# Kernel tuning notes

Measured on AMD Instinct MI355X. Metric: run time of the kernel, lower is better.

## Reference

```python
import jax, jax.numpy as jnp
import numpy as np

T, B, S = 200, 64, 8
D, R, Z, H = 128, 512, 256, 1024
CCOV, CH = 16, 64
DT = 0.05
LAMBDA = 1.0
LOG2PI = float(np.log(2.0 * np.pi))


def _mlp(x, w1, b1, w2, b2):
    return jax.nn.relu(x @ w1 + b1) @ w2 + b2


def setup_inputs() -> dict:
    key = jax.random.key(0)
    ks = jax.random.split(key, 24)
    sc = 0.02
    inp = {
        "X": jax.random.normal(ks[0], (T, B, D), jnp.float32),
        "M": jax.random.uniform(ks[1], (T, B, D), jnp.float32),
        "cov": jax.random.normal(ks[2], (B, CCOV), jnp.float32),
        "path_h": jax.random.normal(ks[3], (T, B, R), jnp.float32),
        "path_hpos": jax.random.normal(ks[4], (T, B, R), jnp.float32),
        "noise": jax.random.normal(ks[5], (T, B, S, Z), jnp.float32),
        # drift MLP: (R+Z) -> H -> Z (tanh applied in reference)
        "drift_w1": jax.random.normal(ks[6], (R + Z, H), jnp.float32) * sc,
        "drift_b1": jnp.zeros((H,), jnp.float32),
        "drift_w2": jax.random.normal(ks[7], (H, Z), jnp.float32) * sc,
        "drift_b2": jnp.zeros((Z,), jnp.float32),
        # diffusion MLP: R -> H -> Z (exp applied in reference)
        "diff_w1": jax.random.normal(ks[8], (R, H), jnp.float32) * sc,
        "diff_b1": jnp.zeros((H,), jnp.float32),
        "diff_w2": jax.random.normal(ks[9], (H, Z), jnp.float32) * sc,
        "diff_b2": jnp.zeros((Z,), jnp.float32),
        # decoder p MLP: (R+Z) -> H -> D
        "p_w1": jax.random.normal(ks[10], (R + Z, H), jnp.float32) * sc,
        "p_b1": jnp.zeros((H,), jnp.float32),
        "p_w2": jax.random.normal(ks[11], (H, D), jnp.float32) * sc,
        "p_b2": jnp.zeros((D,), jnp.float32),
        # covariates SDE map: CCOV -> CH -> Z (tanh applied in reference)
        "cov_w1": jax.random.normal(ks[12], (CCOV, CH), jnp.float32) * sc,
        "cov_b1": jnp.zeros((CH,), jnp.float32),
        "cov_w2": jax.random.normal(ks[13], (CH, Z), jnp.float32) * sc,
        "cov_b2": jnp.zeros((Z,), jnp.float32),
    }
    return inp


def reference(X, M, cov, path_h, path_hpos, noise,
              drift_w1, drift_b1, drift_w2, drift_b2,
              diff_w1, diff_b1, diff_w2, diff_b2,
              p_w1, p_b1, p_w2, p_b2,
              cov_w1, cov_b1, cov_w2, cov_b2):
    dt = DT
    sqrt_dt = np.sqrt(DT).astype(np.float32)
    nB = X.shape[1]

    # z0: covariates_sde_map(cov) repeated over num_samples -> [B, S, Z]
    z0 = jnp.tanh(_mlp(cov, cov_w1, cov_b1, cov_w2, cov_b2))  # [B, Z]
    z0 = jnp.broadcast_to(z0[:, None, :], (nB, S, Z)) * 1.0  # [B, S, Z]

    def step(z, inp):
        h, hpos, Xt, Mrow, eps = inp
        hb = jnp.broadcast_to(h[:, None, :], (nB, S, R))      # prior hidden
        hpb = jnp.broadcast_to(hpos[:, None, :], (nB, S, R))  # posterior hidden

        prior_drift = 0.1 * jnp.tanh(_mlp(jnp.concatenate([hb, z], -1),
                                          drift_w1, drift_b1, drift_w2, drift_b2))
        poster_drift = 0.1 * jnp.tanh(_mlp(jnp.concatenate([hpb, z], -1),
                                           drift_w1, drift_b1, drift_w2, drift_b2))
        diffusion = jnp.exp(_mlp(hb, diff_w1, diff_b1, diff_w2, diff_b2))

        # Euler-Maruyama with posterior drift (train=True path)
        z_new = z + dt * poster_drift + sqrt_dt * diffusion * eps

        # detached min-max normalization over state dim
        z_max = jax.lax.stop_gradient(jnp.max(z_new, -1, keepdims=True))
        z_min = jax.lax.stop_gradient(jnp.min(z_new, -1, keepdims=True))
        z_new = (z_new - z_min) / (z_max - z_min)

        p = _mlp(jnp.concatenate([hb, z_new], -1), p_w1, p_b1, p_w2, p_b2)  # [B,S,D]

        Mt = jnp.mean(Mrow, -1, keepdims=True)  # [B,1]
        errors = (prior_drift - poster_drift) / diffusion
        kld_t = 0.5 * dt * jnp.sum(jnp.mean(errors ** 2, axis=1)) / nB

        # Gaussian NLL with logvar = 0
        nll = 0.5 * (LOG2PI + (Xt[:, None, :] - p) ** 2)  # [B,S,D]
        recon_t = jnp.mean(jnp.sum(jnp.mean(nll, axis=1) * Mt, axis=-1))
        return z_new, (kld_t, recon_t)

    z_final, (klds, recons) = jax.lax.scan(step, z0, (path_h, path_hpos, X, M, noise))
    loss_kld = jnp.sum(klds)
    loss_recon = jnp.sum(recons)
    loss_total = loss_recon + LAMBDA * loss_kld
    return z_final, loss_total, loss_recon, loss_kld
```

## Files before the change

kernel.cpp:

```cpp
#include <hip/hip_runtime.h>
#include <cstddef>
#include <cstdint>

#define T_STEPS 200
#define BB 64
#define SS 8
#define DD 128
#define RR 512
#define ZZ 256
#define HH 1024
#define DT 0.05f
#define SQRT_DT 0.22360679774997896f
#define LOG2PIF 1.8378770664093453f

typedef __attribute__((ext_vector_type(8))) short bf16x8;
typedef __attribute__((ext_vector_type(8))) unsigned short u16x8;
typedef __attribute__((ext_vector_type(4))) float f32x4;
typedef long f8x8;
#define MFMA __builtin_amdgcn_mfma_f32_16x16x32_bf16
#define MFMA8 __builtin_amdgcn_mfma_f32_16x16x32_fp8_fp8

static __device__ __forceinline__ unsigned short f2bf(float x) {
    unsigned int u = __builtin_bit_cast(unsigned int, x);
    u += 0x7fffu + ((u >> 16) & 1u);
    return (unsigned short)(u >> 16);
}
static __device__ __forceinline__ float bf2f(unsigned short h) {
    unsigned int u = ((unsigned int)h) << 16;
    return __builtin_bit_cast(float, u);
}
static __device__ __forceinline__ float fast_tanh(float x) {
    float e = __expf(2.0f * x);
    return 1.0f - 2.0f / (e + 1.0f);
}
static __device__ __forceinline__ unsigned char f2fp8(float x) {
    unsigned int r = 0;
    asm volatile("v_cvt_pk_fp8_f32 %0, %1, %1" : "+v"(r) : "v"(x));
    return (unsigned char)(r & 0xffu);
}
static __device__ __forceinline__ unsigned int f2fp8x4(float a, float b,
                                                      float c, float d) {
    unsigned int p01 = 0, p23 = 0;
    asm volatile("v_cvt_pk_fp8_f32 %0, %1, %2" : "+v"(p01) : "v"(a), "v"(b));
    asm volatile("v_cvt_pk_fp8_f32 %0, %1, %2" : "+v"(p23) : "v"(c), "v"(d));
    return (p01 & 0xffffu) | (p23 << 16);
}

static __device__ __forceinline__ void bar_lds() {
    asm volatile("s_waitcnt lgkmcnt(0)" ::: "memory");
    __builtin_amdgcn_s_barrier();
    __builtin_amdgcn_sched_barrier(0);
}

__global__ void pack_w(const float* __restrict__ src, int K, int N,
                       unsigned short* __restrict__ dst) {
    int total = (K >> 5) * (N >> 4) * 64;
    int p = blockIdx.x * blockDim.x + threadIdx.x;
    if (p >= total) return;
    int lane = p & 63;
    int ksteps = K >> 5;
    int ks = (p >> 6) % ksteps;
    int nt = p / (ksteps << 6);
    int n = (nt << 4) + (lane & 15);
    int k0 = (ks << 5) + ((lane >> 4) << 3);
    uint4 u4;
    unsigned short* tmp = reinterpret_cast<unsigned short*>(&u4);
    for (int i = 0; i < 8; ++i) tmp[i] = f2bf(src[(size_t)(k0 + i) * N + n]);
    *reinterpret_cast<uint4*>(dst + (size_t)p * 8) = u4;
}

__global__ void pack_w_fp8(const float* __restrict__ src, int K, int N,
                           unsigned char* __restrict__ dst) {
    int total = (K >> 5) * (N >> 4) * 64;
    int p = blockIdx.x * blockDim.x + threadIdx.x;
    if (p >= total) return;
    int lane = p & 63;
    int ksteps = K >> 5;
    int ks = (p >> 6) % ksteps;
    int nt = p / (ksteps << 6);
    int n = (nt << 4) + (lane & 15);
    int k0 = (ks << 5) + ((lane >> 4) << 3);
    unsigned long long acc = 0ull;
    for (int i = 0; i < 8; ++i)
        acc |= (unsigned long long)f2fp8(src[(size_t)(k0 + i) * N + n]) << (8 * i);
    *reinterpret_cast<unsigned long long*>(dst + (size_t)p * 8) = acc;
}

__global__ void mt_kernel(const float* __restrict__ M, float* __restrict__ Mt) {
    int wv = (blockIdx.x * blockDim.x + threadIdx.x) >> 6;
    int lane = threadIdx.x & 63;
    if (wv >= T_STEPS * BB) return;
    const float* row = M + (size_t)wv * DD;
    float s = row[lane] + row[lane + 64];
    for (int off = 32; off; off >>= 1) s += __shfl_down(s, off, 64);
    if (lane == 0) Mt[wv] = s * (1.0f / DD);
}

#define PC_GEMM_1024(Asrc, Bp, biasArr, EMIT)                                    \
    {                                                                            \
        f32x4 acc[16];                                                           \
        f32x4 z4 = {0.f, 0.f, 0.f, 0.f};                                        \
        for (int ntl = 0; ntl < 16; ++ntl) acc[ntl] = z4;                        \
        for (int ks = 0; ks < 16; ++ks) {                                        \
            bf16x8 a = *(const bf16x8*)&Asrc[l][(ks << 5) + (q << 3)];           \
            for (int ntl = 0; ntl < 16; ++ntl) {                                 \
                int ntg = (w << 4) + ntl;                                        \
                bf16x8 bb = *(const bf16x8*)(Bp +                                \
                             (((size_t)ntg * 16 + ks) * 64 + lane) * 8);         \
                acc[ntl] = MFMA(a, bb, acc[ntl], 0, 0, 0);                       \
            }                                                                    \
        }                                                                        \
        for (int ntl = 0; ntl < 16; ++ntl) {                                     \
            int n = (((w << 4) + ntl) << 4) + l;                                 \
            float bv = biasArr[n];                                               \
            for (int i = 0; i < 4; ++i) {                                        \
                int rr = (q << 2) + i;                                           \
                float v = acc[ntl][i] + bv;                                      \
                EMIT;                                                            \
            }                                                                    \
        }                                                                        \
    }

#define SCAN_PERM(n) (((n) & ~127) | (((n) & 15) << 3) | (((n) >> 4) & 7))

__global__ __launch_bounds__(256)
void precompute_kernel(const float* __restrict__ h, const float* __restrict__ hpos,
                       const float* __restrict__ b1d, const float* __restrict__ b1p,
                       const float* __restrict__ b1f, const float* __restrict__ b2f,
                       const unsigned short* __restrict__ W1h_p,
                       const unsigned short* __restrict__ PW1h_p,
                       const unsigned short* __restrict__ DW1_p,
                       const unsigned short* __restrict__ DW2_p,
                       unsigned short* __restrict__ HprojQ,
                       unsigned short* __restrict__ HpprojQ,
                       unsigned short* __restrict__ PprojQ,
                       float* __restrict__ DiffQ) {
    __shared__ unsigned short Ahh[16][RR + 8];
    __shared__ unsigned short Ahp[16][RR + 8];
    __shared__ unsigned short Adh[16][HH + 8];
    const int tid = threadIdx.x;
    const int lane = tid & 63;
    const int w = tid >> 6;
    const int q = lane >> 4;
    const int l = lane & 15;
    const int r0 = blockIdx.x << 4;

    for (int idx = tid; idx < (RR << 4); idx += 256) {
        int r = idx >> 9, c = idx & (RR - 1);
        Ahh[r][c] = f2bf(h[(size_t)(r0 + r) * RR + c]);
        Ahp[r][c] = f2bf(hpos[(size_t)(r0 + r) * RR + c]);
    }
    __syncthreads();

    PC_GEMM_1024(Ahh, W1h_p,  b1d,
                 (HprojQ [(size_t)(r0 + rr) * HH + SCAN_PERM(n)] = f2bf(v)));
    PC_GEMM_1024(Ahp, W1h_p,  b1d,
                 (HpprojQ[(size_t)(r0 + rr) * HH + SCAN_PERM(n)] = f2bf(v)));
    PC_GEMM_1024(Ahh, PW1h_p, b1p, (PprojQ [(size_t)(r0 + rr) * HH + n] = f2bf(v)));
    PC_GEMM_1024(Ahh, DW1_p,  b1f, (Adh[rr][n] = f2bf(fmaxf(v, 0.f))));
    __syncthreads();

    {
        f32x4 acc[4];
        f32x4 z4 = {0.f, 0.f, 0.f, 0.f};
        for (int ntl = 0; ntl < 4; ++ntl) acc[ntl] = z4;
        for (int ks = 0; ks < 32; ++ks) {
            bf16x8 a = *(const bf16x8*)&Adh[l][(ks << 5) + (q << 3)];
            for (int ntl = 0; ntl < 4; ++ntl) {
                int ntg = (w << 2) + ntl;
                bf16x8 bb = *(const bf16x8*)(DW2_p +
                             (((size_t)ntg * 32 + ks) * 64 + lane) * 8);
                acc[ntl] = MFMA(a, bb, acc[ntl], 0, 0, 0);
            }
        }
        for (int ntl = 0; ntl < 4; ++ntl) {
            int n = (((w << 2) + ntl) << 4) + l;
            float bv = b2f[n];
            for (int i = 0; i < 4; ++i) {
                int rr = (q << 2) + i;
                DiffQ[(size_t)(r0 + rr) * ZZ + n] = __expf(acc[ntl][i] + bv);
            }
        }
    }
}

__global__ __launch_bounds__(512, 2)
void scan_kernel(const float* __restrict__ cov, const float* __restrict__ noise,
                 const float* __restrict__ b2d,
                 const float* __restrict__ cw1, const float* __restrict__ cb1,
                 const float* __restrict__ cw2, const float* __restrict__ cb2,
                 const unsigned char* __restrict__ W1z_f8,
                 const unsigned char* __restrict__ W2_f8,
                 const unsigned short* __restrict__ HpprojQ,
                 const unsigned short* __restrict__ HprojQ,
                 const float* __restrict__ DiffQ,
                 unsigned short* __restrict__ zhist,
                 float* __restrict__ out,
                 float* __restrict__ loss) {
    __shared__ __align__(16) long W2L[256][64];
    __shared__ __align__(8) unsigned char Az8[8][272];
    __shared__ __align__(8) unsigned char Ah8[16][1032];
    __shared__ __align__(16) float zf[8][256];
    __shared__ float ch[64];

    const int tid = threadIdx.x;
    const int lane = tid & 63;
    const int w = tid >> 6;
    const int q = lane >> 4;
    const int l = lane & 15;
    const int b = blockIdx.x;

    f8x8 w1r[8][8];
    #pragma unroll
    for (int ntl = 0; ntl < 8; ++ntl)
        #pragma unroll
        for (int ks = 0; ks < 8; ++ks)
            w1r[ntl][ks] = *(const f8x8*)(W1z_f8 +
                ((((size_t)(w * 8 + ntl) * 8 + ks) * 64 + lane) << 3));
    f8x8 w2r[32];
    #pragma unroll
    for (int ks = 0; ks < 32; ++ks)
        w2r[ks] = *(const f8x8*)(W2_f8 +
            ((((size_t)(w * 2) * 32 + ks) * 64 + lane) << 3));
    #pragma unroll
    for (int ks = 0; ks < 32; ++ks)
        W2L[w * 32 + ks][lane] = *(const long*)(W2_f8 +
            ((((size_t)(w * 2 + 1) * 32 + ks) * 64 + lane) << 3));

    if (tid < 64) {
        float s = cb1[tid];
        for (int c = 0; c < 16; ++c) s += cov[b * 16 + c] * cw1[c * 64 + tid];
        ch[tid] = fmaxf(s, 0.f);
    }
    __syncthreads();
    if (tid < ZZ) {
        float v = cb2[tid];
        for (int j = 0; j < 64; ++j) v += ch[j] * cw2[j * ZZ + tid];
        v = fast_tanh(v);
        unsigned short hv = f2bf(v);
        unsigned char zb = f2fp8(v);
        for (int s = 0; s < SS; ++s) {
            zf[s][tid] = v;
            Az8[s][tid] = zb;
            zhist[((size_t)b * SS + s) * ZZ + tid] = hv;
        }
    }

    const int colA = (w << 5) + l;
    const int colB = colA + 16;
    float b2dA = b2d[colA], b2dB = b2d[colB];
    float kacc = 0.f;

    float epsA[4], epsB[4], difA = 0.f, difB = 0.f;
    u16x8 hpr;
#define LOAD_SCALARS(TI)                                                        \
    do {                                                                        \
        const size_t tb_ = (size_t)(TI) * BB + b;                               \
        const unsigned short* ps_ = (q < 2) ? HpprojQ : HprojQ;                 \
        hpr = *(const u16x8*)&ps_[tb_ * HH + (w << 7) + (l << 3)];              \
        if (q < 2) {                                                            \
            _Pragma("unroll")                                                   \
            for (int i = 0; i < 4; ++i) {                                       \
                epsA[i] = noise[((tb_ << 3) + (q << 2) + i) * ZZ + colA];       \
                epsB[i] = noise[((tb_ << 3) + (q << 2) + i) * ZZ + colB];       \
            }                                                                   \
            difA = DiffQ[tb_ * ZZ + colA];                                      \
            difB = DiffQ[tb_ * ZZ + colB];                                      \
        }                                                                       \
    } while (0)

    LOAD_SCALARS(0);
    __syncthreads();

    for (int t = 0; t < T_STEPS; ++t) {
        f8x8 a1f[8];
        #pragma unroll
        for (int ks = 0; ks < 8; ++ks)
            a1f[ks] = *(const f8x8*)&Az8[l & 7][(ks << 5) + (q << 3)];
        #pragma unroll
        for (int h = 0; h < 2; ++h) {
            f32x4 acc[4];
            {
                f32x4 z4 = {0.f, 0.f, 0.f, 0.f};
                #pragma unroll
                for (int j = 0; j < 4; ++j) acc[j] = z4;
            }
            #pragma unroll
            for (int ks = 0; ks < 8; ++ks) {
                #pragma unroll
                for (int j = 0; j < 4; ++j)
                    acc[j] = MFMA8(a1f[ks], w1r[h * 4 + j][ks], acc[j], 0, 0, 0);
            }
            #pragma unroll
            for (int j = 0; j < 4; ++j) {
                int ntl = h * 4 + j;
                int n = (w * 8 + ntl) * 16 + l;
                float hp = bf2f(hpr[ntl]);
                #pragma unroll
                for (int i = 0; i < 4; ++i)
                    Ah8[(q << 2) + i][n] = f2fp8(fmaxf(hp + acc[j][i], 0.f));
            }
        }
        bar_lds();

        f32x4 aA[2], aB[2];
        {
            f32x4 z4 = {0.f, 0.f, 0.f, 0.f};
            aA[0] = z4; aA[1] = z4; aB[0] = z4; aB[1] = z4;
        }
        #pragma unroll
        for (int ks = 0; ks < 32; ++ks) {
            f8x8 a2 = *(const f8x8*)&Ah8[l][(ks << 5) + (q << 3)];
            f8x8 bB = (f8x8)W2L[w * 32 + ks][lane];
            aA[ks & 1] = MFMA8(a2, w2r[ks], aA[ks & 1], 0, 0, 0);
            aB[ks & 1] = MFMA8(a2, bB, aB[ks & 1], 0, 0, 0);
        }
        #pragma unroll
        for (int i = 0; i < 4; ++i) {
            float poA = 0.1f * fast_tanh(aA[0][i] + aA[1][i] + b2dA);
            float poB = 0.1f * fast_tanh(aB[0][i] + aB[1][i] + b2dB);
            float prA = __shfl_xor(poA, 32, 64);
            float prB = __shfl_xor(poB, 32, 64);
            if (q < 2) {
                int s = (q << 2) + i;
                float eA = (prA - poA) / difA;
                float eB = (prB - poB) / difB;
                kacc += eA * eA + eB * eB;
                zf[s][colA] += DT * poA + SQRT_DT * difA * epsA[i];
                zf[s][colB] += DT * poB + SQRT_DT * difB * epsB[i];
            }
        }
        if (t + 1 < T_STEPS) LOAD_SCALARS(t + 1);
        bar_lds();

        {
            float4 vv = *(const float4*)&zf[w][lane << 2];
            float mn = fminf(fminf(vv.x, vv.y), fminf(vv.z, vv.w));
            float mx = fmaxf(fmaxf(vv.x, vv.y), fmaxf(vv.z, vv.w));
            for (int off = 32; off; off >>= 1) {
                mn = fminf(mn, __shfl_xor(mn, off, 64));
                mx = fmaxf(mx, __shfl_xor(mx, off, 64));
            }
            float sc = 1.0f / (mx - mn);
            vv.x = (vv.x - mn) * sc; vv.y = (vv.y - mn) * sc;
            vv.z = (vv.z - mn) * sc; vv.w = (vv.w - mn) * sc;
            *(float4*)&zf[w][lane << 2] = vv;
            *(unsigned int*)&Az8[w][lane << 2] = f2fp8x4(vv.x, vv.y, vv.z, vv.w);
            ushort4 hv4;
            hv4.x = f2bf(vv.x); hv4.y = f2bf(vv.y);
            hv4.z = f2bf(vv.z); hv4.w = f2bf(vv.w);
            size_t zo = ((size_t)(t + 1) * BB + b) * (SS * ZZ) + (size_t)w * ZZ;
            *reinterpret_cast<ushort4*>(zhist + zo + (lane << 2)) = hv4;
        }
        bar_lds();
    }
    __syncthreads();

    for (int idx = tid; idx < SS * ZZ; idx += 512) {
        int s = idx >> 8, n = idx & 255;
        out[((size_t)b * SS + s) * ZZ + n] = zf[s][n];
    }

    for (int off = 32; off; off >>= 1) kacc += __shfl_down(kacc, off, 64);
    if (lane == 0) ch[w] = kacc;
    __syncthreads();
    if (tid == 0) {
        float K = 0.f;
        for (int i = 0; i < 8; ++i) K += ch[i];
        float kc = K * (0.5f * DT / (SS * BB));
        atomicAdd(loss + 0, kc);
        atomicAdd(loss + 2, kc);
    }
#undef LOAD_SCALARS
}

__global__ __launch_bounds__(512, 4)
void post_dec(const unsigned short* __restrict__ zhist,
              const unsigned short* __restrict__ PprojQ,
              const float* __restrict__ X, const float* __restrict__ MtQ,
              const float* __restrict__ b2p,
              const unsigned short* __restrict__ PW1z_p,
              const unsigned short* __restrict__ PW2_p,
              float* __restrict__ loss) {
    __shared__ unsigned short Az[4][16][ZZ + 8];
    __shared__ unsigned short Hp[4][16][136];
    __shared__ unsigned short ProjS[8][128];
    __shared__ float b2p_s[DD];
    __shared__ float red[8];
    const int tid = threadIdx.x;
    const int lane = tid & 63;
    const int w = tid >> 6;
    const int q = lane >> 4;
    const int l = lane & 15;
    const int rt = w & 3;
    const int half = w >> 2;
    const int p0 = blockIdx.x << 3;

    for (int idx = tid; idx < 4096; idx += 512) {
        int r = idx >> 6, c4 = (idx & 63) << 2;
        *(ushort4*)&Az[r >> 4][r & 15][c4] =
            *(const ushort4*)&zhist[((size_t)(p0 + BB) * SS + r) * ZZ + c4];
    }
    if (tid < DD) b2p_s[tid] = b2p[tid];

    f32x4 pacc[4];
    {
        f32x4 z4 = {0.f, 0.f, 0.f, 0.f};
        #pragma unroll
        for (int j = 0; j < 4; ++j) pacc[j] = z4;
    }

    for (int nc = 0; nc < 8; ++nc) {
        if (tid < 256) {
            int pair = tid >> 5, c4 = (tid & 31) << 2;
            *(ushort4*)&ProjS[pair][c4] =
                *(const ushort4*)&PprojQ[(size_t)(p0 + pair) * HH + nc * 128 + c4];
        }
        __syncthreads();

        f32x4 za[4];
        {
            f32x4 z4 = {0.f, 0.f, 0.f, 0.f};
            #pragma unroll
            for (int j = 0; j < 4; ++j) za[j] = z4;
        }
        {
            const unsigned short* wb = PW1z_p + lane * 8;
            bf16x8 wq[4];
            #pragma unroll
            for (int f = 0; f < 4; ++f) {
                int ks = f >> 2, j = f & 3;
                wq[f] = *(const bf16x8*)(wb +
                    ((size_t)((nc * 8 + half * 4 + j) * 8 + ks)) * 512);
            }
            #pragma unroll
            for (int f = 0; f < 32; ++f) {
                int ks = f >> 2, j = f & 3;
                bf16x8 a = *(const bf16x8*)&Az[rt][l][(ks << 5) + (q << 3)];
                za[j] = MFMA(a, wq[f & 3], za[j], 0, 0, 0);
                if (f < 28) {
                    int f2 = f + 4, ks2 = f2 >> 2, j2 = f2 & 3;
                    wq[f & 3] = *(const bf16x8*)(wb +
                        ((size_t)((nc * 8 + half * 4 + j2) * 8 + ks2)) * 512);
                }
            }
        }
        #pragma unroll
        for (int j = 0; j < 4; ++j) {
            int c = (half * 4 + j) * 16 + l;
            #pragma unroll
            for (int i = 0; i < 4; ++i) {
                int r = (q << 2) + i;
                int pair = ((rt << 4) + r) >> 3;
                Hp[rt][r][c] = f2bf(fmaxf(bf2f(ProjS[pair][c]) + za[j][i], 0.f));
            }
        }
        __syncthreads();

        {
            const unsigned short* wb2 = PW2_p + lane * 8;
            bf16x8 wq2[4];
            #pragma unroll
            for (int f = 0; f < 4; ++f) {
                int kk = f >> 2, j = f & 3;
                wq2[f] = *(const bf16x8*)(wb2 +
                    ((size_t)((half * 4 + j) * 32 + nc * 4 + kk)) * 512);
            }
            #pragma unroll
            for (int f = 0; f < 16; ++f) {
                int kk = f >> 2, j = f & 3;
                bf16x8 a = *(const bf16x8*)&Hp[rt][l][(kk << 5) + (q << 3)];
                pacc[j] = MFMA(a, wq2[f & 3], pacc[j], 0, 0, 0);
                if (f < 12) {
                    int f2 = f + 4, kk2 = f2 >> 2, j2 = f2 & 3;
                    wq2[f & 3] = *(const bf16x8*)(wb2 +
                        ((size_t)((half * 4 + j2) * 32 + nc * 4 + kk2)) * 512);
                }
            }
        }
        __syncthreads();
    }

    float rl = 0.f;
    #pragma unroll
    for (int j = 0; j < 4; ++j) {
        int n = ((half << 2) + j) * 16 + l;
        float bias = b2p_s[n];
        #pragma unroll
        for (int i = 0; i < 4; ++i) {
            int r = (rt << 4) + (q << 2) + i;
            int pair = p0 + (r >> 3);
            float p = pacc[j][i] + bias;
            float d = X[(size_t)pair * DD + n] - p;
            rl += (0.5f * (LOG2PIF + d * d)) * MtQ[pair];
        }
    }
    rl *= 1.0f / (SS * BB);
    for (int off = 32; off; off >>= 1) rl += __shfl_down(rl, off, 64);
    if (lane == 0) red[w] = rl;
    __syncthreads();
    if (tid == 0) {
        float R = 0.f;
        for (int i = 0; i < 8; ++i) R += red[i];
        atomicAdd(loss + 0, R);
        atomicAdd(loss + 1, R);
    }
}

extern "C" void kernel_launch(void* const* d_in, const int* in_sizes, int n_in,
                              void* d_out, int out_size, void* d_ws, size_t ws_size,
                              hipStream_t stream) {
    (void)in_sizes; (void)n_in; (void)ws_size;
    const float* X         = (const float*)d_in[0];
    const float* M         = (const float*)d_in[1];
    const float* cov       = (const float*)d_in[2];
    const float* path_h    = (const float*)d_in[3];
    const float* path_hpos = (const float*)d_in[4];
    const float* noise     = (const float*)d_in[5];
    const float* drift_w1  = (const float*)d_in[6];
    const float* drift_b1  = (const float*)d_in[7];
    const float* drift_w2  = (const float*)d_in[8];
    const float* drift_b2  = (const float*)d_in[9];
    const float* diff_w1   = (const float*)d_in[10];
    const float* diff_b1   = (const float*)d_in[11];
    const float* diff_w2   = (const float*)d_in[12];
    const float* diff_b2   = (const float*)d_in[13];
    const float* p_w1      = (const float*)d_in[14];
    const float* p_b1      = (const float*)d_in[15];
    const float* p_w2      = (const float*)d_in[16];
    const float* p_b2      = (const float*)d_in[17];
    const float* cov_w1    = (const float*)d_in[18];
    const float* cov_b1    = (const float*)d_in[19];
    const float* cov_w2    = (const float*)d_in[20];
    const float* cov_b2    = (const float*)d_in[21];

    char* ws = (char*)d_ws;
    size_t off = 0;
    auto alloc = [&](size_t bytes) {
        void* p = ws + off;
        off = (off + bytes + 255) & ~(size_t)255;
        return p;
    };
    unsigned short* HprojQ  = (unsigned short*)alloc((size_t)T_STEPS * BB * HH * 2);
    unsigned short* HpprojQ = (unsigned short*)alloc((size_t)T_STEPS * BB * HH * 2);
    unsigned short* PprojQ  = (unsigned short*)alloc((size_t)T_STEPS * BB * HH * 2);
    float*          DiffQ   = (float*)alloc((size_t)T_STEPS * BB * ZZ * 4);
    float*          MtQ     = (float*)alloc((size_t)T_STEPS * BB * 4);
    unsigned short* zhist   = (unsigned short*)alloc((size_t)(T_STEPS + 1) * BB * SS * ZZ * 2);
    unsigned short* PW1z_p  = (unsigned short*)alloc((size_t)ZZ * HH * 2);
    unsigned short* PW2_p   = (unsigned short*)alloc((size_t)HH * DD * 2);
    unsigned short* W1h_p   = (unsigned short*)alloc((size_t)RR * HH * 2);
    unsigned short* PW1h_p  = (unsigned short*)alloc((size_t)RR * HH * 2);
    unsigned short* DW1_p   = (unsigned short*)alloc((size_t)RR * HH * 2);
    unsigned short* DW2_p   = (unsigned short*)alloc((size_t)HH * ZZ * 2);
    unsigned char*  W1z_f8  = (unsigned char*)alloc((size_t)ZZ * HH);
    unsigned char*  W2_f8   = (unsigned char*)alloc((size_t)HH * ZZ);

    hipMemsetAsync(d_out, 0, (size_t)out_size * sizeof(float), stream);

    auto packLaunch = [&](const float* src, int K, int N, unsigned short* dst) {
        int total = (K / 32) * (N / 16) * 64;
        pack_w<<<(total + 255) / 256, 256, 0, stream>>>(src, K, N, dst);
    };
    auto packLaunch8 = [&](const float* src, int K, int N, unsigned char* dst) {
        int total = (K / 32) * (N / 16) * 64;
        pack_w_fp8<<<(total + 255) / 256, 256, 0, stream>>>(src, K, N, dst);
    };
    packLaunch(p_w1 + (size_t)RR * HH,     ZZ, HH, PW1z_p);
    packLaunch(p_w2,                       HH, DD, PW2_p);
    packLaunch(drift_w1, RR, HH, W1h_p);
    packLaunch(p_w1,     RR, HH, PW1h_p);
    packLaunch(diff_w1,  RR, HH, DW1_p);
    packLaunch(diff_w2,  HH, ZZ, DW2_p);
    packLaunch8(drift_w1 + (size_t)RR * HH, ZZ, HH, W1z_f8);
    packLaunch8(drift_w2,                   HH, ZZ, W2_f8);

    mt_kernel<<<(T_STEPS * BB * 64) / 256, 256, 0, stream>>>(M, MtQ);

    precompute_kernel<<<(T_STEPS * BB) / 16, 256, 0, stream>>>(
        path_h, path_hpos, drift_b1, p_b1, diff_b1, diff_b2,
        W1h_p, PW1h_p, DW1_p, DW2_p, HprojQ, HpprojQ, PprojQ, DiffQ);

    float* outp = (float*)d_out;
    float* loss = outp + (size_t)BB * SS * ZZ;

    scan_kernel<<<BB, 512, 0, stream>>>(
        cov, noise, drift_b2, cov_w1, cov_b1, cov_w2, cov_b2,
        W1z_f8, W2_f8, HpprojQ, HprojQ, DiffQ, zhist, outp, loss);

    post_dec<<<(T_STEPS * BB) / 8, 512, 0, stream>>>(
        zhist, PprojQ, X, MtQ, p_b2, PW1z_p, PW2_p, loss);
}
```

Measured before the change: 1.557 ms.

## Merge scan and decoder into persistent kernel with progress-flag producer/consumer overlap

Fuses the sequential scan kernel and the post-decoder kernel into one launch. 64 blocks run the SDE scan and publish per-batch progress counters every 32 steps, while 192 extra blocks poll those counters and decode/compute the reconstruction loss for completed timesteps concurrently. This hides the decoder work behind the latency-bound scan, at the cost of a larger shared memory footprint (one 158KB buffer for both roles, limiting occupancy). It also relies on all 256 blocks being co-resident; if the consumer blocks spin while producer blocks cannot be scheduled, the kernel could stall.

Measured after the change: 1.554 ms. No clear change (-0.2%).

```diff
diff --git a/kernel.cpp b/kernel.cpp
--- a/kernel.cpp
+++ b/kernel.cpp
@@ -185,7 +185,7 @@
 }
 
 __global__ __launch_bounds__(512, 2)
-void scan_kernel(const float* __restrict__ cov, const float* __restrict__ noise,
+void mega_kernel(const float* __restrict__ cov, const float* __restrict__ noise,
                  const float* __restrict__ b2d,
                  const float* __restrict__ cw1, const float* __restrict__ cb1,
                  const float* __restrict__ cw2, const float* __restrict__ cb2,
@@ -196,63 +196,72 @@
                  const float* __restrict__ DiffQ,
                  unsigned short* __restrict__ zhist,
                  float* __restrict__ out,
-                 float* __restrict__ loss) {
-    __shared__ __align__(16) long W2L[256][64];
-    __shared__ __align__(8) unsigned char Az8[8][272];
-    __shared__ __align__(8) unsigned char Ah8[16][1032];
-    __shared__ __align__(16) float zf[8][256];
-    __shared__ float ch[64];
+                 float* __restrict__ loss,
+                 const unsigned short* __restrict__ PprojQ,
+                 const float* __restrict__ X, const float* __restrict__ MtQ,
+                 const float* __restrict__ b2p,
+                 const unsigned short* __restrict__ PW1z_p,
+                 const unsigned short* __restrict__ PW2_p,
+                 unsigned int* __restrict__ progress) {
+    __shared__ __align__(16) char smem[158208];
 
     const int tid = threadIdx.x;
     const int lane = tid & 63;
     const int w = tid >> 6;
     const int q = lane >> 4;
     const int l = lane & 15;
-    const int b = blockIdx.x;
-
-    f8x8 w1r[8][8];
-    #pragma unroll
-    for (int ntl = 0; ntl < 8; ++ntl)
+
+    if (blockIdx.x < BB) {
+        long (*W2L)[64]            = reinterpret_cast<long(*)[64]>(smem);
+        unsigned char (*Az8)[272]  = reinterpret_cast<unsigned char(*)[272]>(smem + 131072);
+        unsigned char (*Ah8)[1032] = reinterpret_cast<unsigned char(*)[1032]>(smem + 133248);
+        float (*zf)[256]           = reinterpret_cast<float(*)[256]>(smem + 149760);
+        float* ch                  = reinterpret_cast<float*>(smem + 157952);
+        const int b = blockIdx.x;
+
+        f8x8 w1r[8][8];
         #pragma unroll
-        for (int ks = 0; ks < 8; ++ks)
-            w1r[ntl][ks] = *(const f8x8*)(W1z_f8 +
-                ((((size_t)(w * 8 + ntl) * 8 + ks) * 64 + lane) << 3));
-    f8x8 w2r[32];
-    #pragma unroll
-    for (int ks = 0; ks < 32; ++ks)
-        w2r[ks] = *(const f8x8*)(W2_f8 +
-            ((((size_t)(w * 2) * 32 + ks) * 64 + lane) << 3));
-    #pragma unroll
-    for (int ks = 0; ks < 32; ++ks)
-        W2L[w * 32 + ks][lane] = *(const long*)(W2_f8 +
-            ((((size_t)(w * 2 + 1) * 32 + ks) * 64 + lane) << 3));
-
-    if (tid < 64) {
-        float s = cb1[tid];
-        for (int c = 0; c < 16; ++c) s += cov[b * 16 + c] * cw1[c * 64 + tid];
-        ch[tid] = fmaxf(s, 0.f);
-    }
-    __syncthreads();
-    if (tid < ZZ) {
-        float v = cb2[tid];
-        for (int j = 0; j < 64; ++j) v += ch[j] * cw2[j * ZZ + tid];
-        v = fast_tanh(v);
-        unsigned short hv = f2bf(v);
-        unsigned char zb = f2fp8(v);
-        for (int s = 0; s < SS; ++s) {
-            zf[s][tid] = v;
-            Az8[s][tid] = zb;
-            zhist[((size_t)b * SS + s) * ZZ + tid] = hv;
-        }
-    }
-
-    const int colA = (w << 5) + l;
-    const int colB = colA + 16;
-    float b2dA = b2d[colA], b2dB = b2d[colB];
-    float kacc = 0.f;
-
-    float epsA[4], epsB[4], difA = 0.f, difB = 0.f;
-    u16x8 hpr;
+        for (int ntl = 0; ntl < 8; ++ntl)
+            #pragma unroll
+            for (int ks = 0; ks < 8; ++ks)
+                w1r[ntl][ks] = *(const f8x8*)(W1z_f8 +
+                    ((((size_t)(w * 8 + ntl) * 8 + ks) * 64 + lane) << 3));
+        f8x8 w2r[32];
+        #pragma unroll
+        for (int ks = 0; ks < 32; ++ks)
+            w2r[ks] = *(const f8x8*)(W2_f8 +
+                ((((size_t)(w * 2) * 32 + ks) * 64 + lane) << 3));
+        #pragma unroll
+        for (int ks = 0; ks < 32; ++ks)
+            W2L[w * 32 + ks][lane] = *(const long*)(W2_f8 +
+                ((((size_t)(w * 2 + 1) * 32 + ks) * 64 + lane) << 3));
+
+        if (tid < 64) {
+            float s = cb1[tid];
+            for (int c = 0; c < 16; ++c) s += cov[b * 16 + c] * cw1[c * 64 + tid];
+            ch[tid] = fmaxf(s, 0.f);
+        }
+        __syncthreads();
+        if (tid < ZZ) {
+            float v = cb2[tid];
+            for (int j = 0; j < 64; ++j) v += ch[j] * cw2[j * ZZ + tid];
+            v = fast_tanh(v);
+            unsigned short hv = f2bf(v);
+            unsigned char zb = f2fp8(v);
+            for (int s = 0; s < SS; ++s) {
+                zf[s][tid] = v;
+                Az8[s][tid] = zb;
+                zhist[((size_t)b * SS + s) * ZZ + tid] = hv;
+            }
+        }
+
+        const int colA = (w << 5) + l;
+        const int colB = colA + 16;
+        float b2dA = b2d[colA], b2dB = b2d[colB];
+        float kacc = 0.f;
+
+        float epsA[4], epsB[4], difA = 0.f, difB = 0.f;
+        u16x8 hpr;
 #define LOAD_SCALARS(TI)                                                        \
     do {                                                                        \
         const size_t tb_ = (size_t)(TI) * BB + b;                               \
@@ -269,241 +278,259 @@
         }                                                                       \
     } while (0)
 
-    LOAD_SCALARS(0);
-    __syncthreads();
-
-    for (int t = 0; t < T_STEPS; ++t) {
-        f8x8 a1f[8];
-        #pragma unroll
-        for (int ks = 0; ks < 8; ++ks)
-            a1f[ks] = *(const f8x8*)&Az8[l & 7][(ks << 5) + (q << 3)];
-        #pragma unroll
-        for (int h = 0; h < 2; ++h) {
-            f32x4 acc[4];
+        LOAD_SCALARS(0);
+        __syncthreads();
+
+        for (int t = 0; t < T_STEPS; ++t) {
+            f8x8 a1f[8];
+            #pragma unroll
+            for (int ks = 0; ks < 8; ++ks)
+                a1f[ks] = *(const f8x8*)&Az8[l & 7][(ks << 5) + (q << 3)];
+            #pragma unroll
+            for (int h = 0; h < 2; ++h) {
+                f32x4 acc[4];
+                {
+                    f32x4 z4 = {0.f, 0.f, 0.f, 0.f};
+                    #pragma unroll
+                    for (int j = 0; j < 4; ++j) acc[j] = z4;
+                }
+                #pragma unroll
+                for (int ks = 0; ks < 8; ++ks) {
+                    #pragma unroll
+                    for (int j = 0; j < 4; ++j)
+                        acc[j] = MFMA8(a1f[ks], w1r[h * 4 + j][ks], acc[j], 0, 0, 0);
+                }
+                #pragma unroll
+                for (int j = 0; j < 4; ++j) {
+                    int ntl = h * 4 + j;
+                    int n = (w * 8 + ntl) * 16 + l;
+                    float hp = bf2f(hpr[ntl]);
+                    #pragma unroll
+                    for (int i = 0; i < 4; ++i)
+                        Ah8[(q << 2) + i][n] = f2fp8(fmaxf(hp + acc[j][i], 0.f));
+                }
+            }
+            bar_lds();
+
+            f32x4 aA[2], aB[2];
+            {
+                f32x4 z4 = {0.f, 0.f, 0.f, 0.f};
+                aA[0] = z4; aA[1] = z4; aB[0] = z4; aB[1] = z4;
+            }
+            #pragma unroll
+            for (int ks = 0; ks < 32; ++ks) {
+                f8x8 a2 = *(const f8x8*)&Ah8[l][(ks << 5) + (q << 3)];
+                f8x8 bB = (f8x8)W2L[w * 32 + ks][lane];
+                aA[ks & 1] = MFMA8(a2, w2r[ks], aA[ks & 1], 0, 0, 0);
+                aB[ks & 1] = MFMA8(a2, bB, aB[ks & 1], 0, 0, 0);
+            }
+            #pragma unroll
+            for (int i = 0; i < 4; ++i) {
+                float poA = 0.1f * fast_tanh(aA[0][i] + aA[1][i] + b2dA);
+                float poB = 0.1f * fast_tanh(aB[0][i] + aB[1][i] + b2dB);
+                float prA = __shfl_xor(poA, 32, 64);
+                float prB = __shfl_xor(poB, 32, 64);
+                if (q < 2) {
+                    int s = (q << 2) + i;
+                    float eA = (prA - poA) / difA;
+                    float eB = (prB - poB) / difB;
+                    kacc += eA * eA + eB * eB;
+                    zf[s][colA] += DT * poA + SQRT_DT * difA * epsA[i];
+                    zf[s][colB] += DT * poB + SQRT_DT * difB * epsB[i];
+                }
+            }
+            if (t + 1 < T_STEPS) LOAD_SCALARS(t + 1);
+            bar_lds();
+
+            {
+                float4 vv = *(const float4*)&zf[w][lane << 2];
+                float mn = fminf(fminf(vv.x, vv.y), fminf(vv.z, vv.w));
+                float mx = fmaxf(fmaxf(vv.x, vv.y), fmaxf(vv.z, vv.w));
+                for (int off = 32; off; off >>= 1) {
+                    mn = fminf(mn, __shfl_xor(mn, off, 64));
+                    mx = fmaxf(mx, __shfl_xor(mx, off, 64));
+                }
+                float sc = 1.0f / (mx - mn);
+                vv.x = (vv.x - mn) * sc; vv.y = (vv.y - mn) * sc;
+                vv.z = (vv.z - mn) * sc; vv.w = (vv.w - mn) * sc;
+                *(float4*)&zf[w][lane << 2] = vv;
+                *(unsigned int*)&Az8[w][lane << 2] = f2fp8x4(vv.x, vv.y, vv.z, vv.w);
+                ushort4 hv4;
+                hv4.x = f2bf(vv.x); hv4.y = f2bf(vv.y);
+                hv4.z = f2bf(vv.z); hv4.w = f2bf(vv.w);
+                size_t zo = ((size_t)(t + 1) * BB + b) * (SS * ZZ) + (size_t)w * ZZ;
+                *reinterpret_cast<ushort4*>(zhist + zo + (lane << 2)) = hv4;
+            }
+            bar_lds();
+
+            if (((t + 1) & 31) == 0) {
+                __syncthreads();
+                if (tid == 0) {
+                    __threadfence();
+                    __hip_atomic_store(&progress[b], (unsigned)(t + 1),
+                                       __ATOMIC_RELEASE, __HIP_MEMORY_SCOPE_AGENT);
+                }
+            }
+        }
+        __syncthreads();
+        if (tid == 0) {
+            __threadfence();
+            __hip_atomic_store(&progress[b], (unsigned)T_STEPS,
+                               __ATOMIC_RELEASE, __HIP_MEMORY_SCOPE_AGENT);
+        }
+
+        for (int idx = tid; idx < SS * ZZ; idx += 512) {
+            int s = idx >> 8, n = idx & 255;
+            out[((size_t)b * SS + s) * ZZ + n] = zf[s][n];
+        }
+
+        for (int off = 32; off; off >>= 1) kacc += __shfl_down(kacc, off, 64);
+        if (lane == 0) ch[w] = kacc;
+        __syncthreads();
+        if (tid == 0) {
+            float K = 0.f;
+            for (int i = 0; i < 8; ++i) K += ch[i];
+            float kc = K * (0.5f * DT / (SS * BB));
+            atomicAdd(loss + 0, kc);
+            atomicAdd(loss + 2, kc);
+        }
+#undef LOAD_SCALARS
+    } else {
+        unsigned short (*AzD)[16][264] = reinterpret_cast<unsigned short(*)[16][264]>(smem);
+        unsigned short (*HpD)[16][136] = reinterpret_cast<unsigned short(*)[16][136]>(smem + 33792);
+        unsigned short (*ProjS)[128]   = reinterpret_cast<unsigned short(*)[128]>(smem + 51200);
+        float* b2p_s                   = reinterpret_cast<float*>(smem + 53248);
+        float* red                     = reinterpret_cast<float*>(smem + 53760);
+        const int rt = w & 3;
+        const int half = w >> 2;
+        const int cons = blockIdx.x - BB;
+
+        if (tid < DD) b2p_s[tid] = b2p[tid];
+
+        for (int c = cons; c < (T_STEPS * BB) / 8; c += 192) {
+            const int p0 = c << 3;
+            const unsigned tneed = (unsigned)((p0 >> 6) + 1);
+            const int bbase = p0 & 63;
+            if (tid == 0) {
+                for (int j = 0; j < 8; ++j) {
+                    while (__hip_atomic_load(&progress[bbase + j], __ATOMIC_RELAXED,
+                                             __HIP_MEMORY_SCOPE_AGENT) < tneed)
+                        __builtin_amdgcn_s_sleep(4);
+                }
+                __threadfence();
+            }
+            __syncthreads();
+
+            for (int idx = tid; idx < 4096; idx += 512) {
+                int r = idx >> 6, c4 = (idx & 63) << 2;
+                *(ushort4*)&AzD[r >> 4][r & 15][c4] =
+                    *(const ushort4*)&zhist[((size_t)(p0 + BB) * SS + r) * ZZ + c4];
+            }
+
+            f32x4 pacc[4];
             {
                 f32x4 z4 = {0.f, 0.f, 0.f, 0.f};
                 #pragma unroll
-                for (int j = 0; j < 4; ++j) acc[j] = z4;
-            }
-            #pragma unroll
-            for (int ks = 0; ks < 8; ++ks) {
+                for (int j = 0; j < 4; ++j) pacc[j] = z4;
+            }
+
+            for (int nc = 0; nc < 8; ++nc) {
+                if (tid < 256) {
+                    int pair = tid >> 5, c4 = (tid & 31) << 2;
+                    *(ushort4*)&ProjS[pair][c4] =
+                        *(const ushort4*)&PprojQ[(size_t)(p0 + pair) * HH + nc * 128 + c4];
+                }
+                __syncthreads();
+
+                f32x4 za[4];
+                {
+                    f32x4 z4 = {0.f, 0.f, 0.f, 0.f};
+                    #pragma unroll
+                    for (int j = 0; j < 4; ++j) za[j] = z4;
+                }
+                {
+                    const unsigned short* wb = PW1z_p + lane * 8;
+                    bf16x8 wq[4];
+                    #pragma unroll
+                    for (int f = 0; f < 4; ++f) {
+                        int ks = f >> 2, j = f & 3;
+                        wq[f] = *(const bf16x8*)(wb +
+                            ((size_t)((nc * 8 + half * 4 + j) * 8 + ks)) * 512);
+                    }
+                    #pragma unroll
+                    for (int f = 0; f < 32; ++f) {
+                        int ks = f >> 2, j = f & 3;
+                        bf16x8 a = *(const bf16x8*)&AzD[rt][l][(ks << 5) + (q << 3)];
+                        za[j] = MFMA(a, wq[f & 3], za[j], 0, 0, 0);
+                        if (f < 28) {
+                            int f2 = f + 4, ks2 = f2 >> 2, j2 = f2 & 3;
+                            wq[f & 3] = *(const bf16x8*)(wb +
+                                ((size_t)((nc * 8 + half * 4 + j2) * 8 + ks2)) * 512);
+                        }
+                    }
+                }
                 #pragma unroll
-                for (int j = 0; j < 4; ++j)
-                    acc[j] = MFMA8(a1f[ks], w1r[h * 4 + j][ks], acc[j], 0, 0, 0);
-            }
+                for (int j = 0; j < 4; ++j) {
+                    int cc = (half * 4 + j) * 16 + l;
+                    #pragma unroll
+                    for (int i = 0; i < 4; ++i) {
+                        int r = (q << 2) + i;
+                        int pair = ((rt << 4) + r) >> 3;
+                        HpD[rt][r][cc] =
+                            f2bf(fmaxf(bf2f(ProjS[pair][cc]) + za[j][i], 0.f));
+                    }
+                }
+                __syncthreads();
+
+                {
+                    const unsigned short* wb2 = PW2_p + lane * 8;
+                    bf16x8 wq2[4];
+                    #pragma unroll
+                    for (int f = 0; f < 4; ++f) {
+                        int kk = f >> 2, j = f & 3;
+                        wq2[f] = *(const bf16x8*)(wb2 +
+                            ((size_t)((half * 4 + j) * 32 + nc * 4 + kk)) * 512);
+                    }
+                    #pragma unroll
+                    for (int f = 0; f < 16; ++f) {
+                        int kk = f >> 2, j = f & 3;
+                        bf16x8 a = *(const bf16x8*)&HpD[rt][l][(kk << 5) + (q << 3)];
+                        pacc[j] = MFMA(a, wq2[f & 3], pacc[j], 0, 0, 0);
+                        if (f < 12) {
+                            int f2 = f + 4, kk2 = f2 >> 2, j2 = f2 & 3;
+                            wq2[f & 3] = *(const bf16x8*)(wb2 +
+                                ((size_t)((half * 4 + j2) * 32 + nc * 4 + kk2)) * 512);
+                        }
+                    }
+                }
+                __syncthreads();
+            }
+
+            float rl = 0.f;
             #pragma unroll
             for (int j = 0; j < 4; ++j) {
-                int ntl = h * 4 + j;
-                int n = (w * 8 + ntl) * 16 + l;
-                float hp = bf2f(hpr[ntl]);
+                int n = ((half << 2) + j) * 16 + l;
+                float bias = b2p_s[n];
                 #pragma unroll
-                for (int i = 0; i < 4; ++i)
-                    Ah8[(q << 2) + i][n] = f2fp8(fmaxf(hp + acc[j][i], 0.f));
-            }
-        }
-        bar_lds();
-
-        f32x4 aA[2], aB[2];
-        {
-            f32x4 z4 = {0.f, 0.f, 0.f, 0.f};
-            aA[0] = z4; aA[1] = z4; aB[0] = z4; aB[1] = z4;
-        }
-        #pragma unroll
-        for (int ks = 0; ks < 32; ++ks) {
-            f8x8 a2 = *(const f8x8*)&Ah8[l][(ks << 5) + (q << 3)];
-            f8x8 bB = (f8x8)W2L[w * 32 + ks][lane];
-            aA[ks & 1] = MFMA8(a2, w2r[ks], aA[ks & 1], 0, 0, 0);
-            aB[ks & 1] = MFMA8(a2, bB, aB[ks & 1], 0, 0, 0);
-        }
-        #pragma unroll
-        for (int i = 0; i < 4; ++i) {
-            float poA = 0.1f * fast_tanh(aA[0][i] + aA[1][i] + b2dA);
-            float poB = 0.1f * fast_tanh(aB[0][i] + aB[1][i] + b2dB);
-            float prA = __shfl_xor(poA, 32, 64);
-            float prB = __shfl_xor(poB, 32, 64);
-            if (q < 2) {
-                int s = (q << 2) + i;
-                float eA = (prA - poA) / difA;
-                float eB = (prB - poB) / difB;
-                kacc += eA * eA + eB * eB;
-                zf[s][colA] += DT * poA + SQRT_DT * difA * epsA[i];
-                zf[s][colB] += DT * poB + SQRT_DT * difB * epsB[i];
-            }
-        }
-        if (t + 1 < T_STEPS) LOAD_SCALARS(t + 1);
-        bar_lds();
-
-        {
-            float4 vv = *(const float4*)&zf[w][lane << 2];
-            float mn = fminf(fminf(vv.x, vv.y), fminf(vv.z, vv.w));
-            float mx = fmaxf(fmaxf(vv.x, vv.y), fmaxf(vv.z, vv.w));
-            for (int off = 32; off; off >>= 1) {
-                mn = fminf(mn, __shfl_xor(mn, off, 64));
-                mx = fmaxf(mx, __shfl_xor(mx, off, 64));
-            }
-            float sc = 1.0f / (mx - mn);
-            vv.x = (vv.x - mn) * sc; vv.y = (vv.y - mn) * sc;
-            vv.z = (vv.z - mn) * sc; vv.w = (vv.w - mn) * sc;
-            *(float4*)&zf[w][lane << 2] = vv;
-            *(unsigned int*)&Az8[w][lane << 2] = f2fp8x4(vv.x, vv.y, vv.z, vv.w);
-            ushort4 hv4;
-            hv4.x = f2bf(vv.x); hv4.y = f2bf(vv.y);
-            hv4.z = f2bf(vv.z); hv4.w = f2bf(vv.w);
-            size_t zo = ((size_t)(t + 1) * BB + b) * (SS * ZZ) + (size_t)w * ZZ;
-            *reinterpret_cast<ushort4*>(zhist + zo + (lane << 2)) = hv4;
-        }
-        bar_lds();
-    }
-    __syncthreads();
-
-    for (int idx = tid; idx < SS * ZZ; idx += 512) {
-        int s = idx >> 8, n = idx & 255;
-        out[((size_t)b * SS + s) * ZZ + n] = zf[s][n];
-    }
-
-    for (int off = 32; off; off >>= 1) kacc += __shfl_down(kacc, off, 64);
-    if (lane == 0) ch[w] = kacc;
-    __syncthreads();
-    if (tid == 0) {
-        float K = 0.f;
-        for (int i = 0; i < 8; ++i) K += ch[i];
-        float kc = K * (0.5f * DT / (SS * BB));
-        atomicAdd(loss + 0, kc);
-        atomicAdd(loss + 2, kc);
-    }
-#undef LOAD_SCALARS
-}
-
-__global__ __launch_bounds__(512, 4)
-void post_dec(const unsigned short* __restrict__ zhist,
-              const unsigned short* __restrict__ PprojQ,
-              const float* __restrict__ X, const float* __restrict__ MtQ,
-              const float* __restrict__ b2p,
-              const unsigned short* __restrict__ PW1z_p,
-              const unsigned short* __restrict__ PW2_p,
-              float* __restrict__ loss) {
-    __shared__ unsigned short Az[4][16][ZZ + 8];
-    __shared__ unsigned short Hp[4][16][136];
-    __shared__ unsigned short ProjS[8][128];
-    __shared__ float b2p_s[DD];
-    __shared__ float red[8];
-    const int tid = threadIdx.x;
-    const int lane = tid & 63;
-    const int w = tid >> 6;
-    const int q = lane >> 4;
-    const int l = lane & 15;
-    const int rt = w & 3;
-    const int half = w >> 2;
-    const int p0 = blockIdx.x << 3;
-
-    for (int idx = tid; idx < 4096; idx += 512) {
-        int r = idx >> 6, c4 = (idx & 63) << 2;
-        *(ushort4*)&Az[r >> 4][r & 15][c4] =
-            *(const ushort4*)&zhist[((size_t)(p0 + BB) * SS + r) * ZZ + c4];
-    }
-    if (tid < DD) b2p_s[tid] = b2p[tid];
-
-    f32x4 pacc[4];
-    {
-        f32x4 z4 = {0.f, 0.f, 0.f, 0.f};
-        #pragma unroll
-        for (int j = 0; j < 4; ++j) pacc[j] = z4;
-    }
-
-    for (int nc = 0; nc < 8; ++nc) {
-        if (tid < 256) {
-            int pair = tid >> 5, c4 = (tid & 31) << 2;
-            *(ushort4*)&ProjS[pair][c4] =
-                *(const ushort4*)&PprojQ[(size_t)(p0 + pair) * HH + nc * 128 + c4];
-        }
-        __syncthreads();
-
-        f32x4 za[4];
-        {
-            f32x4 z4 = {0.f, 0.f, 0.f, 0.f};
-            #pragma unroll
-            for (int j = 0; j < 4; ++j) za[j] = z4;
-        }
-        {
-            const unsigned short* wb = PW1z_p + lane * 8;
-            bf16x8 wq[4];
-            #pragma unroll
-            for (int f = 0; f < 4; ++f) {
-                int ks = f >> 2, j = f & 3;
-                wq[f] = *(const bf16x8*)(wb +
-                    ((size_t)((nc * 8 + half * 4 + j) * 8 + ks)) * 512);
-            }
-            #pragma unroll
-            for (int f = 0; f < 32; ++f) {
-                int ks = f >> 2, j = f & 3;
-                bf16x8 a = *(const bf16x8*)&Az[rt][l][(ks << 5) + (q << 3)];
-                za[j] = MFMA(a, wq[f & 3], za[j], 0, 0, 0);
-                if (f < 28) {
-                    int f2 = f + 4, ks2 = f2 >> 2, j2 = f2 & 3;
-                    wq[f & 3] = *(const bf16x8*)(wb +
-                        ((size_t)((nc * 8 + half * 4 + j2) * 8 + ks2)) * 512);
-                }
-            }
-        }
-        #pragma unroll
-        for (int j = 0; j < 4; ++j) {
-            int c = (half * 4 + j) * 16 + l;
-            #pragma unroll
-            for (int i = 0; i < 4; ++i) {
-                int r = (q << 2) + i;
-                int pair = ((rt << 4) + r) >> 3;
-                Hp[rt][r][c] = f2bf(fmaxf(bf2f(ProjS[pair][c]) + za[j][i], 0.f));
-            }
-        }
-        __syncthreads();
-
-        {
-            const unsigned short* wb2 = PW2_p + lane * 8;
-            bf16x8 wq2[4];
-            #pragma unroll
-            for (int f = 0; f < 4; ++f) {
-                int kk = f >> 2, j = f & 3;
-                wq2[f] = *(const bf16x8*)(wb2 +
-                    ((size_t)((half * 4 + j) * 32 + nc * 4 + kk)) * 512);
-            }
-            #pragma unroll
-            for (int f = 0; f < 16; ++f) {
-                int kk = f >> 2, j = f & 3;
-                bf16x8 a = *(const bf16x8*)&Hp[rt][l][(kk << 5) + (q << 3)];
-                pacc[j] = MFMA(a, wq2[f & 3], pacc[j], 0, 0, 0);
-                if (f < 12) {
-                    int f2 = f + 4, kk2 = f2 >> 2, j2 = f2 & 3;
-                    wq2[f & 3] = *(const bf16x8*)(wb2 +
-                        ((size_t)((half * 4 + j2) * 32 + nc * 4 + kk2)) * 512);
-                }
-            }
-        }
-        __syncthreads();
-    }
-
-    float rl = 0.f;
-    #pragma unroll
-    for (int j = 0; j < 4; ++j) {
-        int n = ((half << 2) + j) * 16 + l;
-        float bias = b2p_s[n];
-        #pragma unroll
-        for (int i = 0; i < 4; ++i) {
-            int r = (rt << 4) + (q << 2) + i;
-            int pair = p0 + (r >> 3);
-            float p = pacc[j][i] + bias;
-            float d = X[(size_t)pair * DD + n] - p;
-            rl += (0.5f * (LOG2PIF + d * d)) * MtQ[pair];
-        }
-    }
-    rl *= 1.0f / (SS * BB);
-    for (int off = 32; off; off >>= 1) rl += __shfl_down(rl, off, 64);
-    if (lane == 0) red[w] = rl;
-    __syncthreads();
-    if (tid == 0) {
-        float R = 0.f;
-        for (int i = 0; i < 8; ++i) R += red[i];
-        atomicAdd(loss + 0, R);
-        atomicAdd(loss + 1, R);
+                for (int i = 0; i < 4; ++i) {
+                    int r = (rt << 4) + (q << 2) + i;
+                    int pair = p0 + (r >> 3);
+                    float p = pacc[j][i] + bias;
+                    float d = X[(size_t)pair * DD + n] - p;
+                    rl += (0.5f * (LOG2PIF + d * d)) * MtQ[pair];
+                }
+            }
+            rl *= 1.0f / (SS * BB);
+            for (int off = 32; off; off >>= 1) rl += __shfl_down(rl, off, 64);
+            if (lane == 0) red[w] = rl;
+            __syncthreads();
+            if (tid == 0) {
+                float R = 0.f;
+                for (int i = 0; i < 8; ++i) R += red[i];
+                atomicAdd(loss + 0, R);
+                atomicAdd(loss + 1, R);
+            }
+        }
     }
 }
 
@@ -555,8 +582,10 @@
     unsigned short* DW2_p   = (unsigned short*)alloc((size_t)HH * ZZ * 2);
     unsigned char*  W1z_f8  = (unsigned char*)alloc((size_t)ZZ * HH);
     unsigned char*  W2_f8   = (unsigned char*)alloc((size_t)HH * ZZ);
+    unsigned int*   progress= (unsigned int*)alloc((size_t)BB * 4);
 
     hipMemsetAsync(d_out, 0, (size_t)out_size * sizeof(float), stream);
+    hipMemsetAsync(progress, 0, (size_t)BB * 4, stream);
 
     auto packLaunch = [&](const float* src, int K, int N, unsigned short* dst) {
         int total = (K / 32) * (N / 16) * 64;
@@ -584,10 +613,8 @@
     float* outp = (float*)d_out;
     float* loss = outp + (size_t)BB * SS * ZZ;
 
-    scan_kernel<<<BB, 512, 0, stream>>>(
+    mega_kernel<<<BB + 192, 512, 0, stream>>>(
         cov, noise, drift_b2, cov_w1, cov_b1, cov_w2, cov_b2,
-        W1z_f8, W2_f8, HpprojQ, HprojQ, DiffQ, zhist, outp, loss);
-
-    post_dec<<<(T_STEPS * BB) / 8, 512, 0, stream>>>(
-        zhist, PprojQ, X, MtQ, p_b2, PW1z_p, PW2_p, loss);
-}
+        W1z_f8, W2_f8, HpprojQ, HprojQ, DiffQ, zhist, outp, loss,
+        PprojQ, X, MtQ, p_b2, PW1z_p, PW2_p, progress);
+}
```
